# Optimization experiments

Hardware: AMD Instinct MI355X
Metric: run time of the kernel (lower is better)

The kernel has to match this reference:

```python
import jax, jax.numpy as jnp
import numpy as np

DIM = 1024
HEADS = 16
HEAD_DIM = DIM // HEADS
B, N = 2, 2048


def setup_inputs() -> dict:
    key = jax.random.key(0)
    k1, k2, k3, k4 = jax.random.split(key, 4)
    x = jax.random.normal(k1, (B, N, DIM), dtype=jnp.float32)
    # torch Linear weights: shape (out_features, in_features), y = x @ W.T + b
    w_qkv = jax.random.normal(k2, (3 * DIM, DIM), dtype=jnp.float32) * (DIM ** -0.5)
    w_proj = jax.random.normal(k3, (DIM, DIM), dtype=jnp.float32) * (DIM ** -0.5)
    b_proj = jax.random.normal(k4, (DIM,), dtype=jnp.float32) * 0.01
    return {"x": x, "w_qkv": w_qkv, "w_proj": w_proj, "b_proj": b_proj}


def reference(x, w_qkv, w_proj, b_proj):
    Bb, Nn, D = x.shape
    scale = HEAD_DIM ** -0.5
    qkv = x @ w_qkv.T                                # [B, N, 3D]
    qkv = qkv.reshape(Bb, Nn, 3, HEADS, HEAD_DIM)
    qkv = jnp.transpose(qkv, (2, 0, 3, 1, 4))        # [3, B, H, N, hd]
    q, k, v = qkv[0], qkv[1], qkv[2]
    attn = jnp.einsum('bhqd,bhkd->bhqk', q, k) * scale
    attn = jax.nn.softmax(attn, axis=-1)
    out = jnp.einsum('bhqk,bhkd->bhqd', attn, v)     # [B, H, N, hd]
    out = jnp.transpose(out, (0, 2, 1, 3)).reshape(Bb, Nn, D)
    return out @ w_proj.T + b_proj
```

## Files before the change

### kernel.cpp

```cpp
#include <hip/hip_runtime.h>
#include <hip/hip_bf16.h>
#include <cstdint>
#include <cstddef>

using u16 = unsigned short;
using u32 = uint32_t;
using f32x4  = __attribute__((ext_vector_type(4))) float;
using bf16x8 = __attribute__((ext_vector_type(8))) __bf16;
using s16x4  = __attribute__((ext_vector_type(4))) short;

#define D_MODEL 1024
#define N_HEADS 16
#define HD      64
#define SEQ     2048
#define QKV_LD  3072
#define K2SCALE 0.18033688011112042f

__device__ __forceinline__ u16 f2b(float f) {
  union { float f; u32 u; } v; v.f = f;
  u32 r = 0x7FFFu + ((v.u >> 16) & 1u);
  return (u16)((v.u + r) >> 16);
}

__device__ __forceinline__ u32 pkbf16(float a, float b) {
  union { __hip_bfloat162 h; u32 u; } c;
  c.h = __float22bfloat162_rn(float2{a, b});
  return c.u;
}

#define MFMA16(A, B, C) __builtin_amdgcn_mfma_f32_16x16x16bf16_1k(A, B, C, 0, 0, 0)

__device__ __forceinline__ void gld16(const u16* g, u16* l) {
  __builtin_amdgcn_global_load_lds(
      (const __attribute__((address_space(1))) void*)g,
      (__attribute__((address_space(3))) void*)l, 16, 0, 0);
}

__global__ void cast3_bf16(const float* __restrict__ x, const float* __restrict__ wq,
                           const float* __restrict__ wp, u16* __restrict__ dst) {
  int i = blockIdx.x * blockDim.x + threadIdx.x;
  const float* src;
  int off;
  if (blockIdx.x < 4096)      { src = x;  off = 0; }
  else if (blockIdx.x < 7168) { src = wq; off = 4096 * 256; }
  else                        { src = wp; off = 7168 * 256; }
  float4 f = ((const float4*)src)[i - off];
  u32 lo = pkbf16(f.x, f.y), hi = pkbf16(f.z, f.w);
  uint2 o = {lo, hi};
  ((uint2*)dst)[i] = o;
}

template<int OUTMODE, int MT>
__launch_bounds__(256, 3)
__global__ void gemm_nt(const u16* __restrict__ A, const u16* __restrict__ B,
                        u16* __restrict__ Ob, float* __restrict__ Of,
                        const float* __restrict__ bias, int N, int K) {
  __shared__ __attribute__((aligned(16))) u16 sA[2][MT * 32];
  __shared__ __attribute__((aligned(16))) u16 sB[2][128 * 32];

  const int tid  = threadIdx.x;
  const int lane = tid & 63;
  const int w    = tid >> 6;
  const int qd   = lane >> 4;
  const int ln   = lane & 15;
  constexpr int MI = MT / 32;
  const int wm   = (w >> 1) * (MT / 2);
  const int wn   = (w & 1) * 64;
  const int m0   = blockIdx.y * MT;
  const int n0   = blockIdx.x * 128;

  auto stage = [&](int kk, int buf) {
    int k0 = kk * 32;
    #pragma unroll
    for (int c = 0; c < MT / 64; ++c) {
      int sbase = w * MT + c * 64;
      int s = sbase + lane;
      int line = s >> 3, sub = (s & 7) ^ (line & 7);
      int row = line * 2 + (sub >> 2), col = (sub & 3) * 8;
      gld16(A + (size_t)(m0 + row) * K + k0 + col, &sA[buf][sbase * 8]);
    }
    #pragma unroll
    for (int c = 0; c < 2; ++c) {
      int sbase = w * 128 + c * 64;
      int s = sbase + lane;
      int line = s >> 3, sub = (s & 7) ^ (line & 7);
      int row = line * 2 + (sub >> 2), col = (sub & 3) * 8;
      gld16(B + (size_t)(n0 + row) * K + k0 + col, &sB[buf][sbase * 8]);
    }
  };

  f32x4 acc[MI][4] = {};
  const int NK = K >> 5;
  stage(0, 0);

  for (int kk = 0; kk < NK; ++kk) {
    const int cur = kk & 1;
    __syncthreads();
    if (kk + 1 < NK) stage(kk + 1, cur ^ 1);

    bf16x8 af[MI], bfm[4];
    #pragma unroll
    for (int i = 0; i < MI; ++i) {
      int r = wm + i * 16 + ln;
      af[i] = *(const bf16x8*)&sA[cur][(r >> 1) * 64 +
                ((((r & 1) << 5) + qd * 8) ^ (((r >> 1) & 7) << 3))];
    }
    #pragma unroll
    for (int j = 0; j < 4; ++j) {
      int r = wn + j * 16 + ln;
      bfm[j] = *(const bf16x8*)&sB[cur][(r >> 1) * 64 +
                ((((r & 1) << 5) + qd * 8) ^ (((r >> 1) & 7) << 3))];
    }
    #pragma unroll
    for (int i = 0; i < MI; ++i)
      #pragma unroll
      for (int j = 0; j < 4; ++j)
        acc[i][j] = __builtin_amdgcn_mfma_f32_16x16x32_bf16(af[i], bfm[j], acc[i][j], 0, 0, 0);
  }

  #pragma unroll
  for (int i = 0; i < MI; ++i) {
    #pragma unroll
    for (int j = 0; j < 4; ++j) {
      #pragma unroll
      for (int r = 0; r < 4; ++r) {
        int row = m0 + wm + i * 16 + qd * 4 + r;
        int col = n0 + wn + j * 16 + ln;
        float v = acc[i][j][r];
        if (OUTMODE == 0) {
          if (col < D_MODEL) v *= K2SCALE;
          Ob[(size_t)row * N + col] = f2b(v);
        } else {
          Of[(size_t)row * N + col] = v + bias[col];
        }
      }
    }
  }
}

__launch_bounds__(256, 2)
__global__ void attn_kernel(const u16* __restrict__ qkv, u16* __restrict__ outb) {
  __shared__ __attribute__((aligned(16))) u16 smem[32768];
  u16 (*sK)[64 * 64] = (u16(*)[64 * 64])smem;
  u32 (*sVT)[64 * 32] = (u32(*)[64 * 32])(smem + 16384);

  const int tid  = threadIdx.x;
  const int lane = tid & 63;
  const int w    = tid >> 6;
  const int qd   = lane >> 4;
  const int ln   = lane & 15;
  const int qp   = blockIdx.x;
  const int h    = blockIdx.y & 15;
  const int b    = blockIdx.y >> 4;
  const size_t tokbase = (size_t)b * SEQ;
  const int q0   = qp * 128;
  const int qoff = h * HD;
  const int koff = D_MODEL + h * HD;
  const int voff = 2 * D_MODEL + h * HD;

  bf16x8 aq[2][2];
  #pragma unroll
  for (int c2 = 0; c2 < 2; ++c2)
    #pragma unroll
    for (int hf = 0; hf < 2; ++hf)
      aq[c2][hf] = *(const bf16x8*)(qkv + (tokbase + q0 + c2 * 64 + w * 16 + ln) * QKV_LD
                                    + qoff + hf * 32 + qd * 8);

  auto stageK = [&](int kt, int buf) {
    #pragma unroll
    for (int c = 0; c < 2; ++c) {
      int sbase = c * 256 + w * 64;
      int s = sbase + lane;
      int row = s >> 3, sub = (s & 7) ^ (row & 7);
      gld16(qkv + (tokbase + kt * 64 + row) * QKV_LD + koff + sub * 8,
            &sK[buf][sbase * 8]);
    }
  };
  auto loadV = [&](int kt, uint4& va, uint4& vb) {
    int tp = tid & 31, d0 = (tid >> 5) * 8;
    const u16* g0 = qkv + (tokbase + kt * 64 + tp * 2) * QKV_LD + voff + d0;
    va = *(const uint4*)g0;
    vb = *(const uint4*)(g0 + QKV_LD);
  };
  auto writeV = [&](int buf, const uint4& va, const uint4& vb) {
    int tp = tid & 31, d0 = (tid >> 5) * 8;
    const u32* a  = (const u32*)&va;
    const u32* bb = (const u32*)&vb;
    #pragma unroll
    for (int e = 0; e < 4; ++e) {
      sVT[buf][(d0 + 2 * e    ) * 32 + (tp ^ (e << 3)    )] =
          __builtin_amdgcn_perm(bb[e], a[e], 0x05040100u);
      sVT[buf][(d0 + 2 * e + 1) * 32 + (tp ^ (e << 3) ^ 4)] =
          __builtin_amdgcn_perm(bb[e], a[e], 0x07060302u);
    }
  };

  stageK(0, 0); stageK(1, 1);
  uint4 vaA, vbA, vaB, vbB;
  loadV(0, vaA, vbA); writeV(0, vaA, vbA);
  loadV(1, vaB, vbB); writeV(1, vaB, vbB);
  loadV(2, vaA, vbA);
  loadV(3, vaB, vbB);

  f32x4 accOT[2][4] = {};
  float psum[2] = {0.f, 0.f};
  const int tsw = (ln & 7) << 2;
  const int ksw = (ln & 7) << 3;

  for (int S = 0; S < 16; ++S) {
    __syncthreads();
    const int t2 = 2 * S + 2, t3 = 2 * S + 3;
    if (t2 < 32) { stageK(t2, t2 & 3); writeV(t2 & 3, vaA, vbA); }
    if (t3 < 32) { stageK(t3, t3 & 3); writeV(t3 & 3, vaB, vbB); }
    if (2 * S + 4 < 32) loadV(2 * S + 4, vaA, vbA);
    if (2 * S + 5 < 32) loadV(2 * S + 5, vaB, vbB);

    #pragma unroll
    for (int half = 0; half < 2; ++half) {
      const int cur = (2 * S + half) & 3;
      #pragma unroll
      for (int cb = 0; cb < 4; ++cb) {
        bf16x8 ak0 = *(const bf16x8*)&sK[cur][(cb * 16 + ln) * 64 + ((qd * 8) ^ ksw)];
        bf16x8 ak1 = *(const bf16x8*)&sK[cur][(cb * 16 + ln) * 64 + ((32 + qd * 8) ^ ksw)];
        f32x4 st[2];
        __builtin_amdgcn_s_setprio(1);
        #pragma unroll
        for (int c2 = 0; c2 < 2; ++c2) {
          f32x4 z = {0.f, 0.f, 0.f, 0.f};
          f32x4 t = __builtin_amdgcn_mfma_f32_16x16x32_bf16(ak0, aq[c2][0], z, 0, 0, 0);
          st[c2]  = __builtin_amdgcn_mfma_f32_16x16x32_bf16(ak1, aq[c2][1], t, 0, 0, 0);
        }
        __builtin_amdgcn_s_setprio(0);
        s16x4 pf[2];
        #pragma unroll
        for (int c2 = 0; c2 < 2; ++c2) {
          float p0 = __builtin_amdgcn_exp2f(st[c2][0]);
          float p1 = __builtin_amdgcn_exp2f(st[c2][1]);
          float p2 = __builtin_amdgcn_exp2f(st[c2][2]);
          float p3 = __builtin_amdgcn_exp2f(st[c2][3]);
          psum[c2] += (p0 + p1) + (p2 + p3);
          union { u32 d[2]; s16x4 v; } pk;
          pk.d[0] = pkbf16(p0, p1);
          pk.d[1] = pkbf16(p2, p3);
          pf[c2] = pk.v;
        }
        __builtin_amdgcn_s_setprio(1);
        #pragma unroll
        for (int ob = 0; ob < 4; ++ob) {
          s16x4 vf = *(const s16x4*)&sVT[cur][(ob * 16 + ln) * 32
                                             + ((cb * 8 + qd * 2) ^ tsw)];
          accOT[0][ob] = MFMA16(vf, pf[0], accOT[0][ob]);
          accOT[1][ob] = MFMA16(vf, pf[1], accOT[1][ob]);
        }
        __builtin_amdgcn_s_setprio(0);
      }
    }
  }

  #pragma unroll
  for (int c2 = 0; c2 < 2; ++c2) {
    float s = psum[c2];
    s += __shfl_xor(s, 16, 64);
    s += __shfl_xor(s, 32, 64);
    psum[c2] = 1.0f / s;
  }

  u16* sOut = smem;
  __syncthreads();
  #pragma unroll
  for (int c2 = 0; c2 < 2; ++c2)
    #pragma unroll
    for (int ob = 0; ob < 4; ++ob) {
      u32 lo = pkbf16(accOT[c2][ob][0] * psum[c2], accOT[c2][ob][1] * psum[c2]);
      u32 hi = pkbf16(accOT[c2][ob][2] * psum[c2], accOT[c2][ob][3] * psum[c2]);
      ((u32*)sOut)[(c2 * 64 + w * 16 + ln) * 36 + ob * 8 + qd * 2    ] = lo;
      ((u32*)sOut)[(c2 * 64 + w * 16 + ln) * 36 + ob * 8 + qd * 2 + 1] = hi;
    }
  __syncthreads();
  #pragma unroll
  for (int it = 0; it < 4; ++it) {
    int idx = it * 256 + tid;
    int token = idx >> 3, chunk = idx & 7;
    uint4 v = *(const uint4*)&sOut[token * 72 + chunk * 8];
    *(uint4*)&outb[(tokbase + q0 + token) * D_MODEL + h * HD + chunk * 8] = v;
  }
}

extern "C" void kernel_launch(void* const* d_in, const int* in_sizes, int n_in,
                              void* d_out, int out_size, void* d_ws, size_t ws_size,
                              hipStream_t stream) {
  const float* x      = (const float*)d_in[0];
  const float* w_qkv  = (const float*)d_in[1];
  const float* w_proj = (const float*)d_in[2];
  const float* b_proj = (const float*)d_in[3];
  float* out = (float*)d_out;

  u16* ws     = (u16*)d_ws;
  u16* xb     = ws;
  u16* wqkvb  = xb    + (size_t)4096 * 1024;
  u16* wprojb = wqkvb + (size_t)3072 * 1024;
  u16* qkvb   = wprojb + (size_t)1024 * 1024;
  u16* attnb  = qkvb  + (size_t)4096 * 3072;

  cast3_bf16<<<8192, 256, 0, stream>>>(x, w_qkv, w_proj, xb);

  gemm_nt<0, 128><<<dim3(24, 32), 256, 0, stream>>>(xb, wqkvb, qkvb, nullptr, nullptr, 3072, 1024);

  attn_kernel<<<dim3(16, 32), 256, 0, stream>>>(qkvb, attnb);

  gemm_nt<1, 64><<<dim3(8, 64), 256, 0, stream>>>(attnb, wprojb, nullptr, out, b_proj, 1024, 1024);
}
```

Measured before the change: 192.7 us.

## Split attention KV tiles across wave groups, swizzle GEMM block order

```diff
diff --git a/kernel.cpp b/kernel.cpp
--- a/kernel.cpp
+++ b/kernel.cpp
@@ -66,8 +66,13 @@
   constexpr int MI = MT / 32;
   const int wm   = (w >> 1) * (MT / 2);
   const int wn   = (w & 1) * 64;
-  const int m0   = blockIdx.y * MT;
-  const int n0   = blockIdx.x * 128;
+
+  const int nbx = gridDim.x;
+  const int lin = blockIdx.y * nbx + blockIdx.x;
+  const int cpx = (nbx * gridDim.y) >> 3;
+  const int swz = (lin & 7) * cpx + (lin >> 3);
+  const int m0  = (swz / nbx) * MT;
+  const int n0  = (swz % nbx) * 128;
 
   auto stage = [&](int kk, int buf) {
     int k0 = kk * 32;
@@ -141,30 +146,34 @@
 __launch_bounds__(256, 2)
 __global__ void attn_kernel(const u16* __restrict__ qkv, u16* __restrict__ outb) {
   __shared__ __attribute__((aligned(16))) u16 smem[32768];
-  u16 (*sK)[64 * 64] = (u16(*)[64 * 64])smem;
+  u16 (*sK)[64 * 64]  = (u16(*)[64 * 64])smem;
   u32 (*sVT)[64 * 32] = (u32(*)[64 * 32])(smem + 16384);
 
   const int tid  = threadIdx.x;
   const int lane = tid & 63;
   const int w    = tid >> 6;
+  const int grp  = w >> 1;
+  const int wh   = w & 1;
   const int qd   = lane >> 4;
   const int ln   = lane & 15;
-  const int qp   = blockIdx.x;
-  const int h    = blockIdx.y & 15;
-  const int b    = blockIdx.y >> 4;
+  const int bid  = blockIdx.x;
+  const int qp   = bid >> 5;
+  const int bh   = bid & 31;
+  const int h    = bh & 15;
+  const int b    = bh >> 4;
   const size_t tokbase = (size_t)b * SEQ;
   const int q0   = qp * 128;
   const int qoff = h * HD;
   const int koff = D_MODEL + h * HD;
   const int voff = 2 * D_MODEL + h * HD;
 
-  bf16x8 aq[2][2];
+  bf16x8 aq[4][2];
   #pragma unroll
-  for (int c2 = 0; c2 < 2; ++c2)
+  for (int c = 0; c < 4; ++c)
     #pragma unroll
     for (int hf = 0; hf < 2; ++hf)
-      aq[c2][hf] = *(const bf16x8*)(qkv + (tokbase + q0 + c2 * 64 + w * 16 + ln) * QKV_LD
-                                    + qoff + hf * 32 + qd * 8);
+      aq[c][hf] = *(const bf16x8*)(qkv + (tokbase + q0 + wh * 64 + c * 16 + ln) * QKV_LD
+                                   + qoff + hf * 32 + qd * 8);
 
   auto stageK = [&](int kt, int buf) {
     #pragma unroll
@@ -182,107 +191,132 @@
     va = *(const uint4*)g0;
     vb = *(const uint4*)(g0 + QKV_LD);
   };
-  auto writeV = [&](int buf, const uint4& va, const uint4& vb) {
+  auto writeV = [&](u32* vbuf, const uint4& va, const uint4& vb) {
     int tp = tid & 31, d0 = (tid >> 5) * 8;
     const u32* a  = (const u32*)&va;
     const u32* bb = (const u32*)&vb;
     #pragma unroll
     for (int e = 0; e < 4; ++e) {
-      sVT[buf][(d0 + 2 * e    ) * 32 + (tp ^ (e << 3)    )] =
+      vbuf[(d0 + 2 * e    ) * 32 + (tp ^ (e << 3)    )] =
           __builtin_amdgcn_perm(bb[e], a[e], 0x05040100u);
-      sVT[buf][(d0 + 2 * e + 1) * 32 + (tp ^ (e << 3) ^ 4)] =
+      vbuf[(d0 + 2 * e + 1) * 32 + (tp ^ (e << 3) ^ 4)] =
           __builtin_amdgcn_perm(bb[e], a[e], 0x07060302u);
     }
   };
 
   stageK(0, 0); stageK(1, 1);
-  uint4 vaA, vbA, vaB, vbB;
-  loadV(0, vaA, vbA); writeV(0, vaA, vbA);
-  loadV(1, vaB, vbB); writeV(1, vaB, vbB);
-  loadV(2, vaA, vbA);
-  loadV(3, vaB, vbB);
-
-  f32x4 accOT[2][4] = {};
-  float psum[2] = {0.f, 0.f};
+  uint4 va, vb, vc, vd;
+  loadV(0, va, vb); writeV(sVT[0], va, vb);
+  loadV(1, vc, vd); writeV(sVT[1], vc, vd);
+  loadV(2, va, vb);
+  loadV(3, vc, vd);
+
+  f32x4 accOT[4][4] = {};
+  float psum[4] = {0.f, 0.f, 0.f, 0.f};
   const int tsw = (ln & 7) << 2;
   const int ksw = (ln & 7) << 3;
 
   for (int S = 0; S < 16; ++S) {
     __syncthreads();
     const int t2 = 2 * S + 2, t3 = 2 * S + 3;
-    if (t2 < 32) { stageK(t2, t2 & 3); writeV(t2 & 3, vaA, vbA); }
-    if (t3 < 32) { stageK(t3, t3 & 3); writeV(t3 & 3, vaB, vbB); }
-    if (2 * S + 4 < 32) loadV(2 * S + 4, vaA, vbA);
-    if (2 * S + 5 < 32) loadV(2 * S + 5, vaB, vbB);
-
-    #pragma unroll
-    for (int half = 0; half < 2; ++half) {
-      const int cur = (2 * S + half) & 3;
-      #pragma unroll
-      for (int cb = 0; cb < 4; ++cb) {
-        bf16x8 ak0 = *(const bf16x8*)&sK[cur][(cb * 16 + ln) * 64 + ((qd * 8) ^ ksw)];
-        bf16x8 ak1 = *(const bf16x8*)&sK[cur][(cb * 16 + ln) * 64 + ((32 + qd * 8) ^ ksw)];
-        f32x4 st[2];
-        __builtin_amdgcn_s_setprio(1);
+    if (t2 < 32) { stageK(t2, t2 & 3); writeV(sVT[t2 & 3], va, vb); }
+    if (t3 < 32) { stageK(t3, t3 & 3); writeV(sVT[t3 & 3], vc, vd); }
+    if (t2 + 2 < 32) loadV(t2 + 2, va, vb);
+    if (t3 + 2 < 32) loadV(t3 + 2, vc, vd);
+
+    const int cur = (2 * S + grp) & 3;
+    #pragma unroll
+    for (int cb = 0; cb < 4; ++cb) {
+      bf16x8 ak0 = *(const bf16x8*)&sK[cur][(cb * 16 + ln) * 64 + ((qd * 8) ^ ksw)];
+      bf16x8 ak1 = *(const bf16x8*)&sK[cur][(cb * 16 + ln) * 64 + ((32 + qd * 8) ^ ksw)];
+      f32x4 st[4];
+      #pragma unroll
+      for (int c = 0; c < 4; ++c) {
+        f32x4 z = {0.f, 0.f, 0.f, 0.f};
+        f32x4 t = __builtin_amdgcn_mfma_f32_16x16x32_bf16(ak0, aq[c][0], z, 0, 0, 0);
+        st[c]   = __builtin_amdgcn_mfma_f32_16x16x32_bf16(ak1, aq[c][1], t, 0, 0, 0);
+      }
+      s16x4 pf[4];
+      #pragma unroll
+      for (int c = 0; c < 4; ++c) {
+        float p0 = __builtin_amdgcn_exp2f(st[c][0]);
+        float p1 = __builtin_amdgcn_exp2f(st[c][1]);
+        float p2 = __builtin_amdgcn_exp2f(st[c][2]);
+        float p3 = __builtin_amdgcn_exp2f(st[c][3]);
+        psum[c] += (p0 + p1) + (p2 + p3);
+        union { u32 d[2]; s16x4 v; } pk;
+        pk.d[0] = pkbf16(p0, p1);
+        pk.d[1] = pkbf16(p2, p3);
+        pf[c] = pk.v;
+      }
+      #pragma unroll
+      for (int ob = 0; ob < 4; ++ob) {
+        s16x4 vf = *(const s16x4*)&sVT[cur][(ob * 16 + ln) * 32
+                                           + ((cb * 8 + qd * 2) ^ tsw)];
         #pragma unroll
-        for (int c2 = 0; c2 < 2; ++c2) {
-          f32x4 z = {0.f, 0.f, 0.f, 0.f};
-          f32x4 t = __builtin_amdgcn_mfma_f32_16x16x32_bf16(ak0, aq[c2][0], z, 0, 0, 0);
-          st[c2]  = __builtin_amdgcn_mfma_f32_16x16x32_bf16(ak1, aq[c2][1], t, 0, 0, 0);
-        }
-        __builtin_amdgcn_s_setprio(0);
-        s16x4 pf[2];
-        #pragma unroll
-        for (int c2 = 0; c2 < 2; ++c2) {
-          float p0 = __builtin_amdgcn_exp2f(st[c2][0]);
-          float p1 = __builtin_amdgcn_exp2f(st[c2][1]);
-          float p2 = __builtin_amdgcn_exp2f(st[c2][2]);
-          float p3 = __builtin_amdgcn_exp2f(st[c2][3]);
-          psum[c2] += (p0 + p1) + (p2 + p3);
-          union { u32 d[2]; s16x4 v; } pk;
-          pk.d[0] = pkbf16(p0, p1);
-          pk.d[1] = pkbf16(p2, p3);
-          pf[c2] = pk.v;
-        }
-        __builtin_amdgcn_s_setprio(1);
-        #pragma unroll
-        for (int ob = 0; ob < 4; ++ob) {
-          s16x4 vf = *(const s16x4*)&sVT[cur][(ob * 16 + ln) * 32
-                                             + ((cb * 8 + qd * 2) ^ tsw)];
-          accOT[0][ob] = MFMA16(vf, pf[0], accOT[0][ob]);
-          accOT[1][ob] = MFMA16(vf, pf[1], accOT[1][ob]);
-        }
-        __builtin_amdgcn_s_setprio(0);
-      }
-    }
-  }
-
+        for (int c = 0; c < 4; ++c)
+          accOT[c][ob] = MFMA16(vf, pf[c], accOT[c][ob]);
+      }
+    }
+  }
+
+  float ps[4];
   #pragma unroll
-  for (int c2 = 0; c2 < 2; ++c2) {
-    float s = psum[c2];
+  for (int c = 0; c < 4; ++c) {
+    float s = psum[c];
     s += __shfl_xor(s, 16, 64);
     s += __shfl_xor(s, 32, 64);
-    psum[c2] = 1.0f / s;
-  }
-
-  u16* sOut = smem;
+    ps[c] = s;
+  }
+
+  float* sPs = (float*)(smem + 28672);
   __syncthreads();
+  if (qd == 0) {
+    #pragma unroll
+    for (int c = 0; c < 4; ++c)
+      sPs[((grp * 2 + wh) * 4 + c) * 16 + ln] = ps[c];
+  }
+  __syncthreads();
+  float pinv[4];
   #pragma unroll
-  for (int c2 = 0; c2 < 2; ++c2)
-    #pragma unroll
-    for (int ob = 0; ob < 4; ++ob) {
-      u32 lo = pkbf16(accOT[c2][ob][0] * psum[c2], accOT[c2][ob][1] * psum[c2]);
-      u32 hi = pkbf16(accOT[c2][ob][2] * psum[c2], accOT[c2][ob][3] * psum[c2]);
-      ((u32*)sOut)[(c2 * 64 + w * 16 + ln) * 36 + ob * 8 + qd * 2    ] = lo;
-      ((u32*)sOut)[(c2 * 64 + w * 16 + ln) * 36 + ob * 8 + qd * 2 + 1] = hi;
-    }
+  for (int c = 0; c < 4; ++c)
+    pinv[c] = 1.0f / (ps[c] + sPs[(((1 - grp) * 2 + wh) * 4 + c) * 16 + ln]);
+
+  float* sAcc = (float*)smem;
+  if (grp == 0) {
+    #pragma unroll
+    for (int c = 0; c < 4; ++c)
+      #pragma unroll
+      for (int ob = 0; ob < 4; ++ob) {
+        f32x4 t = accOT[c][ob] * pinv[c];
+        *(f32x4*)&sAcc[(wh * 64 + c * 16 + ln) * 72 + ob * 16 + qd * 4] = t;
+      }
+  }
   __syncthreads();
-  #pragma unroll
-  for (int it = 0; it < 4; ++it) {
-    int idx = it * 256 + tid;
-    int token = idx >> 3, chunk = idx & 7;
-    uint4 v = *(const uint4*)&sOut[token * 72 + chunk * 8];
-    *(uint4*)&outb[(tokbase + q0 + token) * D_MODEL + h * HD + chunk * 8] = v;
+  if (grp == 1) {
+    #pragma unroll
+    for (int c = 0; c < 4; ++c)
+      #pragma unroll
+      for (int ob = 0; ob < 4; ++ob) {
+        float* p = &sAcc[(wh * 64 + c * 16 + ln) * 72 + ob * 16 + qd * 4];
+        f32x4 t = *(const f32x4*)p;
+        t += accOT[c][ob] * pinv[c];
+        *(f32x4*)p = t;
+      }
+  }
+  __syncthreads();
+
+  {
+    int token = tid >> 1, seg = tid & 1;
+    const float* src = &sAcc[token * 72 + seg * 32];
+    u32 o[16];
+    #pragma unroll
+    for (int e = 0; e < 16; ++e) o[e] = pkbf16(src[2 * e], src[2 * e + 1]);
+    u16* dst = &outb[(tokbase + q0 + token) * D_MODEL + h * HD + seg * 32];
+    *(uint4*)dst        = *(uint4*)&o[0];
+    *(uint4*)(dst + 8)  = *(uint4*)&o[4];
+    *(uint4*)(dst + 16) = *(uint4*)&o[8];
+    *(uint4*)(dst + 24) = *(uint4*)&o[12];
   }
 }
 
@@ -306,7 +340,7 @@
 
   gemm_nt<0, 128><<<dim3(24, 32), 256, 0, stream>>>(xb, wqkvb, qkvb, nullptr, nullptr, 3072, 1024);
 
-  attn_kernel<<<dim3(16, 32), 256, 0, stream>>>(qkvb, attnb);
+  attn_kernel<<<512, 256, 0, stream>>>(qkvb, attnb);
 
   gemm_nt<1, 64><<<dim3(8, 64), 256, 0, stream>>>(attnb, wprojb, nullptr, out, b_proj, 1024, 1024);
 }
```

New measurement: 184.0 us. 1.05x faster.
